# Kernel tuning notes

Hardware: AMD Instinct MI355X
Metric: run time of the kernel (lower is better)

## Reference

```python
import jax, jax.numpy as jnp
import numpy as np

B, N, BS, H, DH, L, FF, V, R = 1, 4096, 64, 12, 64, 4, 3072, 30522, 3
D = H * DH
M = N // BS
NEG = -10000.0


def layernorm(x, g, b, eps=1e-5):
    mu = x.mean(-1, keepdims=True)
    var = ((x - mu) ** 2).mean(-1, keepdims=True)
    return (x - mu) * jax.lax.rsqrt(var + eps) * g + b


def bigbird_attention(q, k, v, band_mask, from_mask, to_mask, blocked_mask, rand_attn):
    # q,k,v: [b,h,n,d]; band_mask [b,1,m-4,BS,3BS]; to_mask [b,1,1,n]; from_mask [b,1,n,1]
    b, h, n, d = q.shape
    m = n // BS
    r = rand_attn.shape[-1]
    sc = 1.0 / jnp.sqrt(jnp.float32(d))
    qb = q.reshape(b, h, m, BS, d)
    kb = k.reshape(b, h, m, BS, d)
    vb = v.reshape(b, h, m, BS, d)
    hid = jnp.arange(h)[:, None, None]
    gk = kb[:, hid, rand_attn].reshape(b, h, m - 2, r * BS, d)  # gathered random keys
    gv = vb[:, hid, rand_attn].reshape(b, h, m - 2, r * BS, d)
    rand_to = blocked_mask[:, rand_attn].reshape(b, h, m - 2, r * BS)
    rand_mask = jnp.einsum('blq,bhlk->bhlqk', blocked_mask[:, 1:-1], rand_to)  # [b,h,m-2,BS,rBS]

    # first block: dense over all keys (global)
    s = jnp.einsum('bhqd,bhkd->bhqk', qb[:, :, 0], k) * sc + (1.0 - to_mask) * NEG
    c_first = jnp.einsum('bhqk,bhkd->bhqd', jax.nn.softmax(s, axis=-1), v)

    # second block: blocks 0,1,2, last, + random row 0
    k2 = jnp.concatenate([kb[:, :, 0], kb[:, :, 1], kb[:, :, 2], kb[:, :, -1], gk[:, :, 0]], axis=2)
    v2 = jnp.concatenate([vb[:, :, 0], vb[:, :, 1], vb[:, :, 2], vb[:, :, -1], gv[:, :, 0]], axis=2)
    s = jnp.einsum('bhqd,bhkd->bhqk', qb[:, :, 1], k2) * sc
    seq_pad = jnp.concatenate([to_mask[..., :3 * BS], to_mask[..., -BS:],
                               jnp.ones((b, 1, 1, r * BS), s.dtype)], axis=3)
    rnd_pad = jnp.concatenate([jnp.ones((b, h, BS, 4 * BS), s.dtype), rand_mask[:, :, 0]], axis=3)
    s = s + (1.0 - jnp.minimum(seq_pad, rnd_pad)) * NEG
    c_second = jnp.einsum('bhqk,bhkd->bhqd', jax.nn.softmax(s, axis=-1), v2)

    # middle blocks: first-global + 3-block band + random + last-global
    mq = qb[:, :, 2:-2]  # [b,h,m-4,BS,d]
    exp_k = jnp.concatenate([kb[:, :, 1:-3], kb[:, :, 2:-2], kb[:, :, 3:-1]], axis=3)
    exp_v = jnp.concatenate([vb[:, :, 1:-3], vb[:, :, 2:-2], vb[:, :, 3:-1]], axis=3)
    inner = jnp.einsum('bhlqd,bhlkd->bhlqk', mq, exp_k) * sc + (1.0 - band_mask) * NEG
    randp = jnp.einsum('bhlqd,bhlkd->bhlqk', mq, gk[:, :, 1:-1]) * sc + (1.0 - rand_mask[:, :, 1:-1]) * NEG
    firstp = jnp.einsum('bhlqd,bhkd->bhlqk', mq, kb[:, :, 0]) * sc + (1.0 - to_mask[:, :, None, :, :BS]) * NEG
    lastp = jnp.einsum('bhlqd,bhkd->bhlqk', mq, kb[:, :, -1]) * sc + (1.0 - to_mask[:, :, None, :, -BS:]) * NEG
    w = jax.nn.softmax(jnp.concatenate([firstp, inner, randp, lastp], axis=-1), axis=-1)
    c_mid = jnp.einsum('bhlqk,bhlkd->bhlqd', w[..., BS:4 * BS], exp_v)
    c_mid = c_mid + jnp.einsum('bhlqk,bhlkd->bhlqd', w[..., 4 * BS:4 * BS + r * BS], gv[:, :, 1:-1])
    c_mid = c_mid + jnp.einsum('bhlqk,bhkd->bhlqd', w[..., :BS], vb[:, :, 0])
    c_mid = c_mid + jnp.einsum('bhlqk,bhkd->bhlqd', w[..., -BS:], vb[:, :, -1])

    # second-to-last block: block 0, last 3 blocks, + random row -1
    k3 = jnp.concatenate([kb[:, :, 0], kb[:, :, -3], kb[:, :, -2], kb[:, :, -1], gk[:, :, -1]], axis=2)
    v3 = jnp.concatenate([vb[:, :, 0], vb[:, :, -3], vb[:, :, -2], vb[:, :, -1], gv[:, :, -1]], axis=2)
    s = jnp.einsum('bhqd,bhkd->bhqk', qb[:, :, -2], k3) * sc
    seq_pad = jnp.concatenate([to_mask[..., :BS], to_mask[..., -3 * BS:],
                               jnp.ones((b, 1, 1, r * BS), s.dtype)], axis=3)
    rnd_pad = jnp.concatenate([jnp.ones((b, h, BS, 4 * BS), s.dtype), rand_mask[:, :, -1]], axis=3)
    s = s + (1.0 - jnp.minimum(seq_pad, rnd_pad)) * NEG
    c_sl = jnp.einsum('bhqk,bhkd->bhqd', jax.nn.softmax(s, axis=-1), v3)

    # last block: dense over all keys (global)
    s = jnp.einsum('bhqd,bhkd->bhqk', qb[:, :, -1], k) * sc + (1.0 - to_mask) * NEG
    c_last = jnp.einsum('bhqk,bhkd->bhqd', jax.nn.softmax(s, axis=-1), v)

    ctx = jnp.concatenate([c_first[:, :, None], c_second[:, :, None], c_mid,
                           c_sl[:, :, None], c_last[:, :, None]], axis=2)
    ctx = ctx.reshape(b, h, n, d) * from_mask
    return ctx.transpose(0, 2, 1, 3).reshape(b, n, h * d)


def forward(input_ids, mask, rand_attn, emb_word, emb_pos, emb_ln_g, emb_ln_b,
            Wq, bq, Wk, bk, Wv, bv, Wo, bo, ln1_g, ln1_b, W1, b1, W2, b2, ln2_g, ln2_b):
    b, n = input_ids.shape
    m = n // BS
    x = emb_word[input_ids] + emb_pos[None, :n]
    x = layernorm(x, emb_ln_g, emb_ln_b)
    blocked_mask = mask.reshape(b, m, BS)
    exp_to = jnp.concatenate([blocked_mask[:, 1:-3], blocked_mask[:, 2:-2], blocked_mask[:, 3:-1]], axis=2)
    band_mask = jnp.einsum('blq,blk->blqk', blocked_mask[:, 2:-2], exp_to)[:, None]
    from_mask = mask.reshape(b, 1, n, 1)
    to_mask = mask.reshape(b, 1, 1, n)
    for i in range(L):
        q = (x @ Wq[i] + bq[i]).reshape(b, n, H, DH).transpose(0, 2, 1, 3)
        k = (x @ Wk[i] + bk[i]).reshape(b, n, H, DH).transpose(0, 2, 1, 3)
        v = (x @ Wv[i] + bv[i]).reshape(b, n, H, DH).transpose(0, 2, 1, 3)
        a = bigbird_attention(q, k, v, band_mask, from_mask, to_mask, blocked_mask, rand_attn)
        a = a @ Wo[i] + bo[i]
        x = layernorm(x + a, ln1_g[i], ln1_b[i])  # dropout is identity in eval
        f = jax.nn.gelu(x @ W1[i] + b1[i], approximate=False) @ W2[i] + b2[i]
        x = layernorm(x + f, ln2_g[i], ln2_b[i])
    return x


def setup_inputs() -> dict:
    key = jax.random.key(0)
    ks = jax.random.split(key, 12)
    s = 0.02
    nrm = lambda k, shape: jax.random.normal(k, shape, jnp.float32) * s
    rng = np.random.default_rng(0)
    rand_attn = jnp.asarray(rng.integers(1, M - 1, size=(H, M - 2, R)), jnp.int32)
    return {
        'input_ids': jax.random.randint(ks[0], (B, N), 0, V),
        'mask': jnp.ones((B, N), jnp.float32),
        'rand_attn': rand_attn,
        'emb_word': nrm(ks[1], (V, D)),
        'emb_pos': nrm(ks[2], (N, D)),
        'emb_ln_g': jnp.ones((D,), jnp.float32), 'emb_ln_b': jnp.zeros((D,), jnp.float32),
        'Wq': nrm(ks[3], (L, D, D)), 'bq': jnp.zeros((L, D), jnp.float32),
        'Wk': nrm(ks[4], (L, D, D)), 'bk': jnp.zeros((L, D), jnp.float32),
        'Wv': nrm(ks[5], (L, D, D)), 'bv': jnp.zeros((L, D), jnp.float32),
        'Wo': nrm(ks[6], (L, D, D)), 'bo': jnp.zeros((L, D), jnp.float32),
        'ln1_g': jnp.ones((L, D), jnp.float32), 'ln1_b': jnp.zeros((L, D), jnp.float32),
        'W1': nrm(ks[7], (L, D, FF)), 'b1': jnp.zeros((L, FF), jnp.float32),
        'W2': nrm(ks[8], (L, FF, D)), 'b2': jnp.zeros((L, D), jnp.float32),
        'ln2_g': jnp.ones((L, D), jnp.float32), 'ln2_b': jnp.zeros((L, D), jnp.float32),
    }


def reference(input_ids, mask, rand_attn, emb_word, emb_pos, emb_ln_g, emb_ln_b,
              Wq, bq, Wk, bk, Wv, bv, Wo, bo, ln1_g, ln1_b, W1, b1, W2, b2, ln2_g, ln2_b):
    return forward(input_ids, mask, rand_attn, emb_word, emb_pos, emb_ln_g, emb_ln_b,
                   Wq, bq, Wk, bk, Wv, bv, Wo, bo, ln1_g, ln1_b, W1, b1, W2, b2, ln2_g, ln2_b)
```

## Files before the change

kernel.cpp:

```cpp
#include <hip/hip_runtime.h>
#include <hip/hip_bf16.h>
#include <math.h>

#define NTOK   4096
#define DMODEL 768
#define NHEAD  12
#define DHEAD  64
#define NLAYER 4
#define DFF    3072
#define NBLK   64
#define NEGC   -10000.0f

using frag8 = __attribute__((ext_vector_type(8))) short;
using f32x4 = __attribute__((ext_vector_type(4))) float;

typedef __attribute__((address_space(3))) void       lds_void;
typedef const __attribute__((address_space(1))) void gbl_void;

__device__ __forceinline__ void gload_lds16(const void* g, void* l) {
  __builtin_amdgcn_global_load_lds((gbl_void*)g, (lds_void*)l, 16, 0, 0);
}

__device__ __forceinline__ float block_sum256(float v) {
  __shared__ float tmp[4];
  #pragma unroll
  for (int o = 32; o > 0; o >>= 1) v += __shfl_down(v, o, 64);
  __syncthreads();
  if ((threadIdx.x & 63) == 0) tmp[threadIdx.x >> 6] = v;
  __syncthreads();
  return tmp[0] + tmp[1] + tmp[2] + tmp[3];
}

__global__ __launch_bounds__(256) void embed_ln_kernel(
    const int* __restrict__ ids, const float* __restrict__ emb_word,
    const float* __restrict__ emb_pos, const float* __restrict__ g,
    const float* __restrict__ b, float* __restrict__ x,
    __hip_bfloat16* __restrict__ xb)
{
  const int n = blockIdx.x;
  const int tid = threadIdx.x;
  const int id = ids[n];
  float v[3];
  #pragma unroll
  for (int j = 0; j < 3; ++j) {
    int d = tid + j * 256;
    v[j] = emb_word[(size_t)id * DMODEL + d] + emb_pos[(size_t)n * DMODEL + d];
  }
  float mu = block_sum256(v[0] + v[1] + v[2]) * (1.0f / DMODEL);
  float var = 0.f;
  #pragma unroll
  for (int j = 0; j < 3; ++j) { float t = v[j] - mu; var += t * t; }
  var = block_sum256(var) * (1.0f / DMODEL);
  float rs = rsqrtf(var + 1e-5f);
  #pragma unroll
  for (int j = 0; j < 3; ++j) {
    int d = tid + j * 256;
    float o = (v[j] - mu) * rs * g[d] + b[d];
    x[(size_t)n * DMODEL + d] = o;
    xb[(size_t)n * DMODEL + d] = (__hip_bfloat16)o;
  }
}

__global__ __launch_bounds__(256) void add_ln_red_kernel(
    const float* __restrict__ xin, const float* __restrict__ P, size_t ps,
    int nparts, const float* __restrict__ bias2,
    const float* __restrict__ g, const float* __restrict__ b,
    float* __restrict__ dst, __hip_bfloat16* __restrict__ dstb)
{
  const int n = blockIdx.x;
  const int tid = threadIdx.x;
  float v[3];
  #pragma unroll
  for (int j = 0; j < 3; ++j) {
    int d = tid + j * 256;
    float s = xin[(size_t)n * DMODEL + d] + bias2[d];
    for (int z = 0; z < nparts; ++z)
      s += P[(size_t)z * ps + (size_t)n * DMODEL + d];
    v[j] = s;
  }
  float mu = block_sum256(v[0] + v[1] + v[2]) * (1.0f / DMODEL);
  float var = 0.f;
  #pragma unroll
  for (int j = 0; j < 3; ++j) { float t = v[j] - mu; var += t * t; }
  var = block_sum256(var) * (1.0f / DMODEL);
  float rs = rsqrtf(var + 1e-5f);
  #pragma unroll
  for (int j = 0; j < 3; ++j) {
    int d = tid + j * 256;
    float ov = (v[j] - mu) * rs * g[d] + b[d];
    dst[(size_t)n * DMODEL + d] = ov;
    dstb[(size_t)n * DMODEL + d] = (__hip_bfloat16)ov;
  }
}

__global__ __launch_bounds__(256) void prep_weights_kernel(
    const float* __restrict__ Wq, const float* __restrict__ Wk,
    const float* __restrict__ Wv, const float* __restrict__ Wo,
    const float* __restrict__ W1, const float* __restrict__ W2,
    const float* __restrict__ bq, const float* __restrict__ bk,
    const float* __restrict__ bv,
    __hip_bfloat16* __restrict__ wqkvT, __hip_bfloat16* __restrict__ woT,
    __hip_bfloat16* __restrict__ w1T, __hip_bfloat16* __restrict__ w2T,
    float* __restrict__ biasf)
{
  const int id = blockIdx.x;
  if (id >= 6912) {
    int t = (id - 6912) * 256 + threadIdx.x;
    if (t < 3 * DMODEL)
      biasf[t] = (t < DMODEL) ? bq[t] : (t < 2 * DMODEL ? bk[t - DMODEL] : bv[t - 2 * DMODEL]);
    return;
  }
  const float* src;
  __hip_bfloat16* dst;
  int K, N, local;
  if (id < 2304) {
    int m = id / 576; local = id % 576;
    src = (m == 0) ? Wq : (m == 1) ? Wk : (m == 2) ? Wv : Wo;
    dst = (m < 3) ? wqkvT + (size_t)m * DMODEL * DMODEL : woT;
    K = DMODEL; N = DMODEL;
  } else if (id < 4608) {
    local = id - 2304; src = W1; dst = w1T; K = DMODEL; N = DFF;
  } else {
    local = id - 4608; src = W2; dst = w2T; K = DFF; N = DMODEL;
  }
  const int ntiles = N / 32;
  const int n0 = (local % ntiles) * 32;
  const int k0 = (local / ntiles) * 32;

  __shared__ float tile[32][33];
  const int c = threadIdx.x & 31;
  const int r0 = threadIdx.x >> 5;
  #pragma unroll
  for (int i = 0; i < 4; ++i) {
    int r = r0 + i * 8;
    tile[r][c] = src[(size_t)(k0 + r) * N + n0 + c];
  }
  __syncthreads();
  #pragma unroll
  for (int i = 0; i < 4; ++i) {
    int r = r0 + i * 8;
    dst[(size_t)(n0 + r) * K + k0 + c] = (__hip_bfloat16)tile[c][r];
  }
}

__global__ __launch_bounds__(512, 2) void gemm256_kernel(
    const __hip_bfloat16* __restrict__ A, int ld,
    const __hip_bfloat16* __restrict__ BT,
    const float* __restrict__ bias,
    float* __restrict__ Cf, size_t cfStride,
    __hip_bfloat16* __restrict__ Cb, int ldC,
    int Kpart, int do_gelu)
{
  __shared__ uint4 smem4[131072 / 16];
  char* lds = (char*)smem4;
  const int tid = threadIdx.x;
  const int bm = blockIdx.x * 256;
  const int bn = blockIdx.y * 256;
  const int z  = blockIdx.z;
  const int wave = tid >> 6, lane = tid & 63;
  const int wm = wave >> 2;
  const int wn = wave & 3;
  const int lm = lane & 15, quad = lane >> 4;

  const int srow = tid >> 3;
  const int schx = ((tid & 7) ^ (srow & 7)) * 16;
  const int ldst0 = tid * 16;
  const int ldst1 = 8192 + tid * 16;
  const size_t koffb = (size_t)z * Kpart * 2;
  const char* Abytes = (const char*)A + koffb;
  const char* Bbytes = (const char*)BT + koffb;
  const size_t ldab = (size_t)ld * 2;

  const int co0 = ((0 + quad) ^ (lm & 7)) * 16;
  const int co1 = ((4 + quad) ^ (lm & 7)) * 16;

  f32x4 acc[8][4];
  #pragma unroll
  for (int i = 0; i < 8; ++i)
    #pragma unroll
    for (int j = 0; j < 4; ++j)
      acc[i][j] = (f32x4){0.f, 0.f, 0.f, 0.f};

#define STAGE(BASE, ROW0, LOFF, KB) do {                                      \
    const char* _s = (BASE) + (size_t)((ROW0) + srow) * ldab + (KB) + schx;   \
    gload_lds16(_s, lds + (LOFF) + ldst0);                                    \
    gload_lds16(_s + 64 * ldab, lds + (LOFF) + ldst1);                        \
  } while (0)

  STAGE(Abytes, bm,        0,             (size_t)0);
  STAGE(Abytes, bm + 128,  16384,         (size_t)0);
  STAGE(Bbytes, bn,        65536,         (size_t)0);
  STAGE(Bbytes, bn + 128,  65536 + 16384, (size_t)0);

  frag8 a[4][2], b[2][2];

#define RD_A(MTB) do {                                                        \
    _Pragma("unroll")                                                         \
    for (int mt = 0; mt < 4; ++mt) {                                          \
      const char* ap = Ab + (size_t)((wm * 128 + ((MTB) + mt) * 16 + lm) * 128); \
      a[mt][0] = *(const frag8*)(ap + co0);                                   \
      a[mt][1] = *(const frag8*)(ap + co1);                                   \
    } } while (0)
#define RD_B(NTB) do {                                                        \
    _Pragma("unroll")                                                         \
    for (int nt = 0; nt < 2; ++nt) {                                          \
      const char* bp = Bb + (size_t)((wn * 64 + ((NTB) + nt) * 16 + lm) * 128); \
      b[nt][0] = *(const frag8*)(bp + co0);                                   \
      b[nt][1] = *(const frag8*)(bp + co1);                                   \
    } } while (0)
#define MMQ(MTB, NTB) do {                                                    \
    _Pragma("unroll")                                                         \
    for (int mt = 0; mt < 4; ++mt)                                            \
      _Pragma("unroll")                                                       \
      for (int nt = 0; nt < 2; ++nt) {                                        \
        acc[(MTB) + mt][(NTB) + nt] = __builtin_amdgcn_mfma_f32_16x16x32_bf16( \
            a[mt][0], b[nt][0], acc[(MTB) + mt][(NTB) + nt], 0, 0, 0);        \
        acc[(MTB) + mt][(NTB) + nt] = __builtin_amdgcn_mfma_f32_16x16x32_bf16( \
            a[mt][1], b[nt][1], acc[(MTB) + mt][(NTB) + nt], 0, 0, 0);        \
      } } while (0)

  const int NT = Kpart >> 6;
  for (int t = 0; t < NT; ++t) {
    const int p = t & 1;
    const char* Ab = lds + p * 32768;
    const char* Bb = lds + 65536 + p * 32768;
    const int qb_ = (p ^ 1) * 32768;
    const size_t kb = (size_t)(t + 1) * 128;
    const bool more = (t + 1 < NT);

    if (more) {
      STAGE(Abytes, bm, qb_, kb);
      asm volatile("s_waitcnt vmcnt(2)" ::: "memory");
    } else {
      asm volatile("s_waitcnt vmcnt(0)" ::: "memory");
    }
    __builtin_amdgcn_sched_barrier(0);
    __builtin_amdgcn_s_barrier();
    __builtin_amdgcn_sched_barrier(0);
    RD_A(0); RD_B(0);
    __builtin_amdgcn_s_setprio(1);
    MMQ(0, 0);
    __builtin_amdgcn_s_setprio(0);
    __builtin_amdgcn_s_barrier();

    RD_B(2);
    if (more) STAGE(Abytes, bm + 128, qb_ + 16384, kb);
    __builtin_amdgcn_s_barrier();
    __builtin_amdgcn_s_setprio(1);
    MMQ(0, 2);
    __builtin_amdgcn_s_setprio(0);
    __builtin_amdgcn_s_barrier();

    RD_A(4);
    if (more) STAGE(Bbytes, bn, 65536 + qb_, kb);
    __builtin_amdgcn_s_barrier();
    __builtin_amdgcn_s_setprio(1);
    MMQ(4, 2);
    __builtin_amdgcn_s_setprio(0);
    __builtin_amdgcn_s_barrier();

    RD_B(0);
    if (more) STAGE(Bbytes, bn + 128, 65536 + qb_ + 16384, kb);
    __builtin_amdgcn_s_barrier();
    __builtin_amdgcn_s_setprio(1);
    MMQ(4, 0);
    __builtin_amdgcn_s_setprio(0);
    __builtin_amdgcn_s_barrier();
  }

#undef STAGE
#undef RD_A
#undef RD_B
#undef MMQ

  float* Cfz = Cf ? Cf + (size_t)z * cfStride : nullptr;
  #pragma unroll
  for (int mt = 0; mt < 8; ++mt)
    #pragma unroll
    for (int nt = 0; nt < 4; ++nt)
      #pragma unroll
      for (int rr = 0; rr < 4; ++rr) {
        int row = bm + wm * 128 + mt * 16 + quad * 4 + rr;
        int col = bn + wn * 64 + nt * 16 + lm;
        float v = acc[mt][nt][rr];
        if (bias) v += bias[col];
        if (do_gelu) v = 0.5f * v * (1.f + erff(v * 0.70710678118654752f));
        if (Cfz) Cfz[(size_t)row * ldC + col] = v;
        if (Cb) Cb[(size_t)row * ldC + col] = (__hip_bfloat16)v;
      }
}

__global__ __launch_bounds__(256) void attn_kernel(
    const __hip_bfloat16* __restrict__ qkvb, const float* __restrict__ mask,
    const int* __restrict__ rand_attn, __hip_bfloat16* __restrict__ outp,
    float* __restrict__ Mpart, float* __restrict__ Lpart, float* __restrict__ Opart)
{
  const int h = blockIdx.x;
  const int item = blockIdx.y;
  const int tid = threadIdx.x;

  int qi, chunk;
  if (item < 8)       { qi = 0;        chunk = item; }
  else if (item < 70) { qi = item - 7; chunk = -1; }
  else                { qi = 63;       chunk = item - 70; }

  __shared__ __hip_bfloat16 Qs[64 * 72];
  __shared__ __hip_bfloat16 Ks[64 * 72];
  __shared__ __hip_bfloat16 VTs[64 * 72];
  __shared__ __hip_bfloat16 Ps[64 * 72];
  __shared__ int slist[8];
  __shared__ int snb;

  const __hip_bfloat16* qg = qkvb;
  const __hip_bfloat16* kg = qkvb + DMODEL;
  const __hip_bfloat16* vg = qkvb + 2 * DMODEL;
  const int ldq = 3 * DMODEL;

  const int wave = tid >> 6, lane = tid & 63;
  const int wm = wave * 16;
  const int lm = lane & 15, quad = lane >> 4;

  {
    int r = tid >> 2, c0 = (tid & 3) * 16;
    const __hip_bfloat16* qp = qg + (size_t)(qi * 64 + r) * ldq + h * 64 + c0;
    uint4 a = *(const uint4*)qp;
    uint4 b = *(const uint4*)(qp + 8);
    *(uint4*)(Qs + r * 72 + c0) = a;
    *(uint4*)(Qs + r * 72 + c0 + 8) = b;
  }
  if (tid == 0) {
    if (chunk >= 0) {
      for (int j = 0; j < 8; ++j) slist[j] = chunk * 8 + j;
      snb = 8;
    } else {
      const int* ra = rand_attn + ((size_t)h * 62 + (qi - 1)) * 3;
      if (qi == 1)       { slist[0] = 0; slist[1] = 1;  slist[2] = 2;  slist[3] = 63; }
      else if (qi == 62) { slist[0] = 0; slist[1] = 61; slist[2] = 62; slist[3] = 63; }
      else               { slist[0] = 0; slist[1] = qi - 1; slist[2] = qi; slist[3] = qi + 1; }
      slist[4] = ra[0]; slist[5] = ra[1]; slist[6] = ra[2];
      int nb = 7;
      if (qi >= 2 && qi <= 61) { slist[7] = 63; nb = 8; }
      snb = nb;
    }
  }
  __syncthreads();
  const int nb = snb;

  frag8 aq0 = *(const frag8*)(Qs + (wm + lm) * 72 + quad * 8);
  frag8 aq1 = *(const frag8*)(Qs + (wm + lm) * 72 + 32 + quad * 8);

  float mold[4], lsum[4];
  #pragma unroll
  for (int r = 0; r < 4; ++r) { mold[r] = -1e30f; lsum[r] = 0.f; }
  f32x4 oacc[4];
  #pragma unroll
  for (int t = 0; t < 4; ++t) oacc[t] = (f32x4){0.f, 0.f, 0.f, 0.f};

  const int sr = tid >> 2, sc0 = (tid & 3) * 16;

  for (int bi = 0; bi < nb; ++bi) {
    const int kb = slist[bi];
    const __hip_bfloat16* kp = kg + (size_t)(kb * 64 + sr) * ldq + h * 64 + sc0;
    const __hip_bfloat16* vp = vg + (size_t)(kb * 64 + sr) * ldq + h * 64 + sc0;
    uint4 kv0 = *(const uint4*)kp;
    uint4 kv1 = *(const uint4*)(kp + 8);
    uint4 vv0 = *(const uint4*)vp;
    uint4 vv1 = *(const uint4*)(vp + 8);
    float msk[4];
    #pragma unroll
    for (int t = 0; t < 4; ++t) msk[t] = mask[kb * 64 + t * 16 + lm];

    __syncthreads();
    *(uint4*)(Ks + sr * 72 + sc0) = kv0;
    *(uint4*)(Ks + sr * 72 + sc0 + 8) = kv1;
    {
      union { uint4 u[2]; __hip_bfloat16 h16[16]; } vu;
      vu.u[0] = vv0; vu.u[1] = vv1;
      #pragma unroll
      for (int j = 0; j < 16; ++j)
        VTs[(sc0 + j) * 72 + sr] = vu.h16[j];
    }
    __syncthreads();

    f32x4 sacc[4];
    #pragma unroll
    for (int t = 0; t < 4; ++t) sacc[t] = (f32x4){0.f, 0.f, 0.f, 0.f};
    #pragma unroll
    for (int t = 0; t < 4; ++t) {
      frag8 bk0 = *(const frag8*)(Ks + (t * 16 + lm) * 72 + quad * 8);
      frag8 bk1 = *(const frag8*)(Ks + (t * 16 + lm) * 72 + 32 + quad * 8);
      sacc[t] = __builtin_amdgcn_mfma_f32_16x16x32_bf16(aq0, bk0, sacc[t], 0, 0, 0);
      sacc[t] = __builtin_amdgcn_mfma_f32_16x16x32_bf16(aq1, bk1, sacc[t], 0, 0, 0);
    }

    float xs[4][4];
    #pragma unroll
    for (int t = 0; t < 4; ++t)
      #pragma unroll
      for (int r = 0; r < 4; ++r)
        xs[t][r] = sacc[t][r] * 0.125f + (1.f - msk[t]) * NEGC;

    float al[4], psum[4];
    #pragma unroll
    for (int r = 0; r < 4; ++r) {
      float rm = fmaxf(fmaxf(xs[0][r], xs[1][r]), fmaxf(xs[2][r], xs[3][r]));
      rm = fmaxf(rm, __shfl_xor(rm, 1, 64));
      rm = fmaxf(rm, __shfl_xor(rm, 2, 64));
      rm = fmaxf(rm, __shfl_xor(rm, 4, 64));
      rm = fmaxf(rm, __shfl_xor(rm, 8, 64));
      float mnew = fmaxf(mold[r], rm);
      al[r] = __expf(mold[r] - mnew);
      float s = 0.f;
      #pragma unroll
      for (int t = 0; t < 4; ++t) {
        float p = __expf(xs[t][r] - mnew);
        xs[t][r] = p;
        s += p;
      }
      s += __shfl_xor(s, 1, 64);
      s += __shfl_xor(s, 2, 64);
      s += __shfl_xor(s, 4, 64);
      s += __shfl_xor(s, 8, 64);
      psum[r] = s;
      mold[r] = mnew;
    }
    #pragma unroll
    for (int r = 0; r < 4; ++r) lsum[r] = lsum[r] * al[r] + psum[r];
    #pragma unroll
    for (int t = 0; t < 4; ++t)
      #pragma unroll
      for (int r = 0; r < 4; ++r)
        oacc[t][r] *= al[r];

    #pragma unroll
    for (int t = 0; t < 4; ++t)
      #pragma unroll
      for (int r = 0; r < 4; ++r)
        Ps[(wm + quad * 4 + r) * 72 + t * 16 + lm] = (__hip_bfloat16)xs[t][r];

    frag8 ap0 = *(const frag8*)(Ps + (wm + lm) * 72 + quad * 8);
    frag8 ap1 = *(const frag8*)(Ps + (wm + lm) * 72 + 32 + quad * 8);
    #pragma unroll
    for (int t = 0; t < 4; ++t) {
      frag8 bv0 = *(const frag8*)(VTs + (t * 16 + lm) * 72 + quad * 8);
      frag8 bv1 = *(const frag8*)(VTs + (t * 16 + lm) * 72 + 32 + quad * 8);
      oacc[t] = __builtin_amdgcn_mfma_f32_16x16x32_bf16(ap0, bv0, oacc[t], 0, 0, 0);
      oacc[t] = __builtin_amdgcn_mfma_f32_16x16x32_bf16(ap1, bv1, oacc[t], 0, 0, 0);
    }
  }

  if (chunk < 0) {
    #pragma unroll
    for (int r = 0; r < 4; ++r) {
      int row = qi * 64 + wm + quad * 4 + r;
      float sc2 = mask[row] / lsum[r];
      #pragma unroll
      for (int t = 0; t < 4; ++t)
        outp[(size_t)row * DMODEL + h * 64 + t * 16 + lm] =
            (__hip_bfloat16)(oacc[t][r] * sc2);
    }
  } else {
    const int idx = (h * 2 + (qi == 63 ? 1 : 0)) * 8 + chunk;
    #pragma unroll
    for (int r = 0; r < 4; ++r) {
      int row = wm + quad * 4 + r;
      #pragma unroll
      for (int t = 0; t < 4; ++t)
        Opart[(size_t)idx * 4096 + row * 64 + t * 16 + lm] = oacc[t][r];
      if (lm == 0) {
        Mpart[idx * 64 + row] = mold[r];
        Lpart[idx * 64 + row] = lsum[r];
      }
    }
  }
}

__global__ __launch_bounds__(256) void attn_merge_kernel(
    const float* __restrict__ Mpart, const float* __restrict__ Lpart,
    const float* __restrict__ Opart, const float* __restrict__ mask,
    __hip_bfloat16* __restrict__ outp)
{
  const int h = blockIdx.x, side = blockIdx.y;
  const int qi = side ? 63 : 0;
  const int tid = threadIdx.x;
  const int r = tid >> 2;
  const int d0 = (tid & 3) * 16;
  const int base = (h * 2 + side) * 8;

  float mv[8], m = -1e30f;
  #pragma unroll
  for (int c = 0; c < 8; ++c) { mv[c] = Mpart[(base + c) * 64 + r]; m = fmaxf(m, mv[c]); }
  float sc[8], l = 0.f;
  #pragma unroll
  for (int c = 0; c < 8; ++c) {
    sc[c] = __expf(mv[c] - m);
    l += Lpart[(base + c) * 64 + r] * sc[c];
  }
  float o[16];
  #pragma unroll
  for (int d = 0; d < 16; ++d) o[d] = 0.f;
  #pragma unroll
  for (int c = 0; c < 8; ++c) {
    const float* Op = Opart + (size_t)(base + c) * 4096 + r * 64 + d0;
    #pragma unroll
    for (int d4 = 0; d4 < 4; ++d4) {
      float4 v4 = *(const float4*)(Op + d4 * 4);
      o[d4 * 4 + 0] += v4.x * sc[c];
      o[d4 * 4 + 1] += v4.y * sc[c];
      o[d4 * 4 + 2] += v4.z * sc[c];
      o[d4 * 4 + 3] += v4.w * sc[c];
    }
  }
  const int row = qi * 64 + r;
  float inv = mask[row] / l;
  #pragma unroll
  for (int d = 0; d < 16; ++d)
    outp[(size_t)row * DMODEL + h * 64 + d0 + d] = (__hip_bfloat16)(o[d] * inv);
}

extern "C" void kernel_launch(void* const* d_in, const int* in_sizes, int n_in,
                              void* d_out, int out_size, void* d_ws, size_t ws_size,
                              hipStream_t stream)
{
  const int*   ids      = (const int*)  d_in[0];
  const float* mask     = (const float*)d_in[1];
  const int*   rand_att = (const int*)  d_in[2];
  const float* emb_word = (const float*)d_in[3];
  const float* emb_pos  = (const float*)d_in[4];
  const float* eg       = (const float*)d_in[5];
  const float* eb       = (const float*)d_in[6];
  const float* Wq = (const float*)d_in[7];
  const float* bq = (const float*)d_in[8];
  const float* Wk = (const float*)d_in[9];
  const float* bk = (const float*)d_in[10];
  const float* Wv = (const float*)d_in[11];
  const float* bv = (const float*)d_in[12];
  const float* Wo = (const float*)d_in[13];
  const float* bo = (const float*)d_in[14];
  const float* ln1g = (const float*)d_in[15];
  const float* ln1b = (const float*)d_in[16];
  const float* W1 = (const float*)d_in[17];
  const float* bf1 = (const float*)d_in[18];
  const float* W2 = (const float*)d_in[19];
  const float* bf2 = (const float*)d_in[20];
  const float* ln2g = (const float*)d_in[21];
  const float* ln2b = (const float*)d_in[22];

  const size_t ND = (size_t)NTOK * DMODEL;
  float* x   = (float*)d_ws;
  __hip_bfloat16* xb = (__hip_bfloat16*)(x + ND);
  float* P   = (float*)(xb + ND);
  __hip_bfloat16* qkvb = (__hip_bfloat16*)(P + 4 * ND);
  __hip_bfloat16* fb_b = qkvb + 3 * ND;
  __hip_bfloat16* ab_b = fb_b + (size_t)NTOK * DFF;
  __hip_bfloat16* wqkvT = ab_b + ND;
  __hip_bfloat16* woT  = wqkvT + (size_t)3 * DMODEL * DMODEL;
  __hip_bfloat16* w1T  = woT  + (size_t)DMODEL * DMODEL;
  __hip_bfloat16* w2T  = w1T  + (size_t)DFF * DMODEL;
  float* biasf = (float*)(w2T + (size_t)DMODEL * DFF);
  float* Mpart = biasf + 3 * DMODEL;
  float* Lpart = Mpart + NHEAD * 2 * 8 * 64;
  float* Opart = Lpart + NHEAD * 2 * 8 * 64;

  embed_ln_kernel<<<NTOK, 256, 0, stream>>>(ids, emb_word, emb_pos, eg, eb, x, xb);

  for (int l = 0; l < NLAYER; ++l) {
    const float* Wq_l = Wq + (size_t)l * DMODEL * DMODEL;
    const float* Wk_l = Wk + (size_t)l * DMODEL * DMODEL;
    const float* Wv_l = Wv + (size_t)l * DMODEL * DMODEL;
    const float* Wo_l = Wo + (size_t)l * DMODEL * DMODEL;
    const float* W1_l = W1 + (size_t)l * DMODEL * DFF;
    const float* W2_l = W2 + (size_t)l * DFF * DMODEL;

    prep_weights_kernel<<<6921, 256, 0, stream>>>(
        Wq_l, Wk_l, Wv_l, Wo_l, W1_l, W2_l,
        bq + (size_t)l * DMODEL, bk + (size_t)l * DMODEL, bv + (size_t)l * DMODEL,
        wqkvT, woT, w1T, w2T, biasf);

    gemm256_kernel<<<dim3(NTOK / 256, 3 * DMODEL / 256), 512, 0, stream>>>(
        xb, DMODEL, wqkvT, biasf, nullptr, 0, qkvb, 3 * DMODEL, DMODEL, 0);

    attn_kernel<<<dim3(NHEAD, 78), 256, 0, stream>>>(qkvb, mask, rand_att, ab_b,
                                                     Mpart, Lpart, Opart);
    attn_merge_kernel<<<dim3(NHEAD, 2), 256, 0, stream>>>(Mpart, Lpart, Opart, mask, ab_b);

    gemm256_kernel<<<dim3(NTOK / 256, DMODEL / 256, 4), 512, 0, stream>>>(
        ab_b, DMODEL, woT, nullptr, P, ND, nullptr, DMODEL, DMODEL / 4, 0);
    add_ln_red_kernel<<<NTOK, 256, 0, stream>>>(x, P, ND, 4, bo + (size_t)l * DMODEL,
                                                ln1g + (size_t)l * DMODEL,
                                                ln1b + (size_t)l * DMODEL, x, xb);

    gemm256_kernel<<<dim3(NTOK / 256, DFF / 256), 512, 0, stream>>>(
        xb, DMODEL, w1T, bf1 + (size_t)l * DFF, nullptr, 0, fb_b, DFF, DMODEL, 1);

    gemm256_kernel<<<dim3(NTOK / 256, DMODEL / 256, 4), 512, 0, stream>>>(
        fb_b, DFF, w2T, nullptr, P, ND, nullptr, DMODEL, DFF / 4, 0);
    add_ln_red_kernel<<<NTOK, 256, 0, stream>>>(x, P, ND, 4, bf2 + (size_t)l * DMODEL,
                                                ln2g + (size_t)l * DMODEL,
                                                ln2b + (size_t)l * DMODEL,
                                                (l == NLAYER - 1) ? (float*)d_out : x, xb);
  }
}
```

Before: 1.190 ms.

## Restructure GEMM main loop: whole-tile prefetch, fewer barriers, XCD-aware tile remap

The 256x256 GEMM now issues all eight global-to-LDS loads for the next K-tile at the start of each iteration instead of spreading them across four barrier-separated phases. That cuts per-iteration barriers from eight to two and keeps two B fragment sets in registers so the MFMA phases run back to back. The workgroup index is also remapped in groups of eight so neighbouring tiles land on the same XCD, aiming at better L2 reuse. In exchange it uses more registers for the extra B fragments and issues loads in a burstier pattern. The remap assumes the tile count divides evenly by eight.

```diff
diff --git a/kernel.cpp b/kernel.cpp
--- a/kernel.cpp
+++ b/kernel.cpp
@@ -151,12 +151,18 @@
     __hip_bfloat16* __restrict__ Cb, int ldC,
     int Kpart, int do_gelu)
 {
-  __shared__ uint4 smem4[131072 / 16];
-  char* lds = (char*)smem4;
+  __shared__ alignas(16) __hip_bfloat16 lds[2][512][64];
   const int tid = threadIdx.x;
-  const int bm = blockIdx.x * 256;
-  const int bn = blockIdx.y * 256;
+
+  const int gx = gridDim.x;
+  const int nwg = gx * gridDim.y;
+  const int cpx = nwg >> 3;
+  const int orig = blockIdx.y * gx + blockIdx.x;
+  const int wg = (orig & 7) * cpx + (orig >> 3);
+  const int bm = (wg % gx) * 256;
+  const int bn = (wg / gx) * 256;
   const int z  = blockIdx.z;
+
   const int wave = tid >> 6, lane = tid & 63;
   const int wm = wave >> 2;
   const int wn = wave & 3;
@@ -164,15 +170,14 @@
 
   const int srow = tid >> 3;
   const int schx = ((tid & 7) ^ (srow & 7)) * 16;
-  const int ldst0 = tid * 16;
-  const int ldst1 = 8192 + tid * 16;
+  const int dcol = (tid & 7) * 8;
   const size_t koffb = (size_t)z * Kpart * 2;
   const char* Abytes = (const char*)A + koffb;
   const char* Bbytes = (const char*)BT + koffb;
   const size_t ldab = (size_t)ld * 2;
 
-  const int co0 = ((0 + quad) ^ (lm & 7)) * 16;
-  const int co1 = ((4 + quad) ^ (lm & 7)) * 16;
+  const int co0e = ((0 + quad) ^ (lm & 7)) * 8;
+  const int co1e = ((4 + quad) ^ (lm & 7)) * 8;
 
   f32x4 acc[8][4];
   #pragma unroll
@@ -181,94 +186,85 @@
     for (int j = 0; j < 4; ++j)
       acc[i][j] = (f32x4){0.f, 0.f, 0.f, 0.f};
 
-#define STAGE(BASE, ROW0, LOFF, KB) do {                                      \
-    const char* _s = (BASE) + (size_t)((ROW0) + srow) * ldab + (KB) + schx;   \
-    gload_lds16(_s, lds + (LOFF) + ldst0);                                    \
-    gload_lds16(_s + 64 * ldab, lds + (LOFF) + ldst1);                        \
+#define STAGE4(BUF, KB) do {                                                  \
+    const char* _a0 = Abytes + (size_t)(bm + srow) * ldab + (KB) + schx;      \
+    gload_lds16(_a0,              &lds[BUF][srow      ][dcol]);               \
+    gload_lds16(_a0 +  64 * ldab, &lds[BUF][srow +  64][dcol]);               \
+    const char* _a1 = _a0 + 128 * ldab;                                       \
+    gload_lds16(_a1,              &lds[BUF][srow + 128][dcol]);               \
+    gload_lds16(_a1 +  64 * ldab, &lds[BUF][srow + 192][dcol]);               \
+    const char* _b0 = Bbytes + (size_t)(bn + srow) * ldab + (KB) + schx;      \
+    gload_lds16(_b0,              &lds[BUF][srow + 256][dcol]);               \
+    gload_lds16(_b0 +  64 * ldab, &lds[BUF][srow + 320][dcol]);               \
+    const char* _b1 = _b0 + 128 * ldab;                                       \
+    gload_lds16(_b1,              &lds[BUF][srow + 384][dcol]);               \
+    gload_lds16(_b1 +  64 * ldab, &lds[BUF][srow + 448][dcol]);               \
   } while (0)
 
-  STAGE(Abytes, bm,        0,             (size_t)0);
-  STAGE(Abytes, bm + 128,  16384,         (size_t)0);
-  STAGE(Bbytes, bn,        65536,         (size_t)0);
-  STAGE(Bbytes, bn + 128,  65536 + 16384, (size_t)0);
-
-  frag8 a[4][2], b[2][2];
-
-#define RD_A(MTB) do {                                                        \
+#define RD_A(LP, MTB, DST) do {                                               \
     _Pragma("unroll")                                                         \
     for (int mt = 0; mt < 4; ++mt) {                                          \
-      const char* ap = Ab + (size_t)((wm * 128 + ((MTB) + mt) * 16 + lm) * 128); \
-      a[mt][0] = *(const frag8*)(ap + co0);                                   \
-      a[mt][1] = *(const frag8*)(ap + co1);                                   \
+      const int rr_ = wm * 128 + ((MTB) + mt) * 16 + lm;                      \
+      DST[mt][0] = *(const frag8*)&lds[LP][rr_][co0e];                        \
+      DST[mt][1] = *(const frag8*)&lds[LP][rr_][co1e];                        \
     } } while (0)
-#define RD_B(NTB) do {                                                        \
+#define RD_B(LP, NTB, DST) do {                                               \
     _Pragma("unroll")                                                         \
     for (int nt = 0; nt < 2; ++nt) {                                          \
-      const char* bp = Bb + (size_t)((wn * 64 + ((NTB) + nt) * 16 + lm) * 128); \
-      b[nt][0] = *(const frag8*)(bp + co0);                                   \
-      b[nt][1] = *(const frag8*)(bp + co1);                                   \
+      const int rr_ = 256 + wn * 64 + ((NTB) + nt) * 16 + lm;                 \
+      DST[nt][0] = *(const frag8*)&lds[LP][rr_][co0e];                        \
+      DST[nt][1] = *(const frag8*)&lds[LP][rr_][co1e];                        \
     } } while (0)
-#define MMQ(MTB, NTB) do {                                                    \
+#define MMQ(MTB, AA, BB, NTB) do {                                            \
     _Pragma("unroll")                                                         \
     for (int mt = 0; mt < 4; ++mt)                                            \
       _Pragma("unroll")                                                       \
       for (int nt = 0; nt < 2; ++nt) {                                        \
         acc[(MTB) + mt][(NTB) + nt] = __builtin_amdgcn_mfma_f32_16x16x32_bf16( \
-            a[mt][0], b[nt][0], acc[(MTB) + mt][(NTB) + nt], 0, 0, 0);        \
+            AA[mt][0], BB[nt][0], acc[(MTB) + mt][(NTB) + nt], 0, 0, 0);      \
         acc[(MTB) + mt][(NTB) + nt] = __builtin_amdgcn_mfma_f32_16x16x32_bf16( \
-            a[mt][1], b[nt][1], acc[(MTB) + mt][(NTB) + nt], 0, 0, 0);        \
+            AA[mt][1], BB[nt][1], acc[(MTB) + mt][(NTB) + nt], 0, 0, 0);      \
       } } while (0)
+
+  STAGE4(0, (size_t)0);
+
+  frag8 a[4][2], b0[2][2], b2[2][2];
 
   const int NT = Kpart >> 6;
   for (int t = 0; t < NT; ++t) {
     const int p = t & 1;
-    const char* Ab = lds + p * 32768;
-    const char* Bb = lds + 65536 + p * 32768;
-    const int qb_ = (p ^ 1) * 32768;
     const size_t kb = (size_t)(t + 1) * 128;
-    const bool more = (t + 1 < NT);
-
-    if (more) {
-      STAGE(Abytes, bm, qb_, kb);
-      asm volatile("s_waitcnt vmcnt(2)" ::: "memory");
+
+    if (t + 1 < NT) {
+      STAGE4(p ^ 1, kb);
+      asm volatile("s_waitcnt vmcnt(8)" ::: "memory");
     } else {
       asm volatile("s_waitcnt vmcnt(0)" ::: "memory");
     }
     __builtin_amdgcn_sched_barrier(0);
     __builtin_amdgcn_s_barrier();
     __builtin_amdgcn_sched_barrier(0);
-    RD_A(0); RD_B(0);
+
+    RD_A(p, 0, a); RD_B(p, 0, b0);
     __builtin_amdgcn_s_setprio(1);
-    MMQ(0, 0);
+    MMQ(0, a, b0, 0);
     __builtin_amdgcn_s_setprio(0);
+    RD_B(p, 2, b2);
+    __builtin_amdgcn_s_setprio(1);
+    MMQ(0, a, b2, 2);
+    __builtin_amdgcn_s_setprio(0);
+    RD_A(p, 4, a);
+    __builtin_amdgcn_s_setprio(1);
+    MMQ(4, a, b2, 2);
+    MMQ(4, a, b0, 0);
+    __builtin_amdgcn_s_setprio(0);
+
+    asm volatile("s_waitcnt lgkmcnt(0)" ::: "memory");
+    __builtin_amdgcn_sched_barrier(0);
     __builtin_amdgcn_s_barrier();
-
-    RD_B(2);
-    if (more) STAGE(Abytes, bm + 128, qb_ + 16384, kb);
-    __builtin_amdgcn_s_barrier();
-    __builtin_amdgcn_s_setprio(1);
-    MMQ(0, 2);
-    __builtin_amdgcn_s_setprio(0);
-    __builtin_amdgcn_s_barrier();
-
-    RD_A(4);
-    if (more) STAGE(Bbytes, bn, 65536 + qb_, kb);
-    __builtin_amdgcn_s_barrier();
-    __builtin_amdgcn_s_setprio(1);
-    MMQ(4, 2);
-    __builtin_amdgcn_s_setprio(0);
-    __builtin_amdgcn_s_barrier();
-
-    RD_B(0);
-    if (more) STAGE(Bbytes, bn + 128, 65536 + qb_ + 16384, kb);
-    __builtin_amdgcn_s_barrier();
-    __builtin_amdgcn_s_setprio(1);
-    MMQ(4, 0);
-    __builtin_amdgcn_s_setprio(0);
-    __builtin_amdgcn_s_barrier();
-  }
-
-#undef STAGE
+  }
+
+#undef STAGE4
 #undef RD_A
 #undef RD_B
 #undef MMQ
```

New measurement: 1.250 ms. 5.0% more time.
